# Kernel optimization log

Measured on AMD Instinct MI355X. Metric: run time of the kernel, lower is better.

## Reference

```python
import jax, jax.numpy as jnp
import numpy as np

RNN = 512        # rnn_units == embedding_units (required by LSTMCell input size)
ATT = 512        # attention_units
FEAT = 512       # feat_chans
VOCAB = 110
V1 = VOCAB + 1
MAX_LEN = 30
STEPS = MAX_LEN + 1
B, H, W = 32, 8, 32


def _lstm_cell(x, h, c, wih, whh, bih, bhh):
    # torch.nn.LSTMCell gate order: i, f, g, o
    gates = x @ wih.T + bih + h @ whh.T + bhh
    i, f, g, o = jnp.split(gates, 4, axis=-1)
    i, f, o = jax.nn.sigmoid(i), jax.nn.sigmoid(f), jax.nn.sigmoid(o)
    g = jnp.tanh(g)
    c_new = f * c + i * g
    h_new = o * jnp.tanh(c_new)
    return h_new, c_new


def setup_inputs() -> dict:
    key = jax.random.key(0)
    ks = jax.random.split(key, 16)
    s = 0.05

    def rn(k, shape):
        return jax.random.normal(k, shape, jnp.float32) * s

    return {
        "features": jax.random.normal(ks[0], (B, FEAT, H, W), jnp.float32),
        "holistic": jax.random.normal(ks[1], (B, RNN), jnp.float32),  # unused by forward (matches torch)
        "gt": jax.random.randint(ks[2], (B, STEPS), 0, V1),
        # AttentionModule params
        "W_feat": rn(ks[3], (ATT, FEAT, 3, 3)),
        "b_feat": jnp.zeros((ATT,), jnp.float32),
        "W_state": rn(ks[4], (ATT, RNN)),     # 1x1 conv, no bias
        "w_att": rn(ks[5], (ATT,)),           # 1x1 conv -> 1 channel, no bias
        # embedding (Linear, no bias): (embedding_units, vocab+1)
        "W_embed": rn(ks[6], (RNN, V1)),
        # LSTM cell 0
        "wih0": rn(ks[7], (4 * RNN, RNN)),
        "whh0": rn(ks[8], (4 * RNN, RNN)),
        "bih0": jnp.zeros((4 * RNN,), jnp.float32),
        "bhh0": jnp.zeros((4 * RNN,), jnp.float32),
        # LSTM cell 1
        "wih1": rn(ks[9], (4 * RNN, RNN)),
        "whh1": rn(ks[10], (4 * RNN, RNN)),
        "bih1": jnp.zeros((4 * RNN,), jnp.float32),
        "bhh1": jnp.zeros((4 * RNN,), jnp.float32),
        # output dense: (vocab+1, 2*rnn_units)
        "W_out": rn(ks[11], (V1, 2 * RNN)),
        "b_out": jnp.zeros((V1,), jnp.float32),
    }


def reference(features, holistic, gt, W_feat, b_feat, W_state, w_att, W_embed,
              wih0, whh0, bih0, bhh0, wih1, whh1, bih1, bhh1, W_out, b_out):
    Bsz, C, Hh, Ww = features.shape
    dt = features.dtype

    # feat_conv(features) is invariant across decode steps -> compute once
    feat_proj = jax.lax.conv_general_dilated(
        features, W_feat, window_strides=(1, 1), padding="SAME",
        dimension_numbers=("NCHW", "OIHW", "NCHW"),
    ) + b_feat[None, :, None, None]  # (B, ATT, H, W)

    # teacher-forced symbols: step 0 uses zeros, step t uses one_hot(gt[:, t-1])
    syms = jnp.concatenate(
        [jnp.zeros((Bsz, 1, V1), dt), jax.nn.one_hot(gt[:, :STEPS - 1], V1, dtype=dt)],
        axis=1,
    )
    syms = jnp.swapaxes(syms, 0, 1)  # (STEPS, B, V1)

    z = jnp.zeros((Bsz, RNN), dt)
    init = (z, z, z, z)  # h0, c0, h1, c1 (torch LSTMCell defaults to zero state)

    def step(carry, sym):
        h0, c0, h1, c1 = carry
        x = sym @ W_embed.T                                  # (B, RNN)
        h0, c0 = _lstm_cell(x, h0, c0, wih0, whh0, bih0, bhh0)
        h1, c1 = _lstm_cell(h0, h1, c1, wih1, whh1, bih1, bhh1)
        # attention glimpse: state is h1 broadcast as a 1x1 feature map
        sp = h1 @ W_state.T                                  # (B, ATT)
        proj = jnp.tanh(feat_proj + sp[:, :, None, None])    # (B, ATT, H, W)
        att = jnp.einsum("bahw,a->bhw", proj, w_att).reshape(Bsz, -1)
        att = jax.nn.softmax(att, axis=1).reshape(Bsz, Hh, Ww)
        glimpse = jnp.einsum("bchw,bhw->bc", features, att)  # (B, FEAT)
        logits = jnp.concatenate([h1, glimpse], axis=1) @ W_out.T + b_out
        return (h0, c0, h1, c1), logits

    _, logits = jax.lax.scan(step, init, syms)               # (STEPS, B, V1)
    return jnp.swapaxes(logits, 0, 1)                        # (B, STEPS, V1)
```

## Files before the change

kernel.cpp:

```cpp
#include <hip/hip_runtime.h>
#include <hip/hip_bf16.h>


#define RNN   512
#define V1    111
#define STEPS 31
#define HWP   256
#define NWG   128

typedef unsigned short ushortT;
typedef unsigned int   uintT;
typedef __attribute__((ext_vector_type(8))) short bf16x8;
typedef __attribute__((ext_vector_type(4))) float f32x4;

__device__ __forceinline__ float blo(uintT u){ union { uintT i; float f; } v; v.i = u << 16; return v.f; }
__device__ __forceinline__ float bhi(uintT u){ union { uintT i; float f; } v; v.i = u & 0xffff0000u; return v.f; }
__device__ __forceinline__ ushortT f2b(float f){
  __hip_bfloat16 h = __float2bfloat16(f);
  union { __hip_bfloat16 b; ushortT s; } v; v.b = h; return v.s;
}
__device__ __forceinline__ uintT packbf(float lo, float hi){
  return (uintT)f2b(lo) | ((uintT)f2b(hi) << 16);
}
__device__ __forceinline__ bf16x8 u4_to_b8(uint4 u){
  union { uint4 a; bf16x8 b; } v; v.a = u; return v.b;
}
__device__ __forceinline__ float sigf(float x){ return 1.f/(1.f + __expf(-x)); }
__device__ __forceinline__ float tanh_f(float x){ float e = __expf(2.f*x); return 1.f - 2.f/(e+1.f); }

__device__ __forceinline__ uintT sload_u(const uintT* p){
  return __hip_atomic_load((uintT*)p, __ATOMIC_RELAXED, __HIP_MEMORY_SCOPE_SYSTEM);
}
__device__ __forceinline__ void sstore_u(uintT* p, uintT v){
  __hip_atomic_store(p, v, __ATOMIC_RELAXED, __HIP_MEMORY_SCOPE_SYSTEM);
}
__device__ __forceinline__ void wait_ge(uintT* p, uintT tgt){
  for (;;){
    if (__hip_atomic_load(p, __ATOMIC_RELAXED, __HIP_MEMORY_SCOPE_SYSTEM) >= tgt) break;
    __builtin_amdgcn_s_sleep(2);
  }
}

__global__ __launch_bounds__(256) void k_pre(const float* __restrict__ feat,
                                             const float* __restrict__ Wf,
                                             uintT* __restrict__ fT,
                                             uintT* __restrict__ wb){
  const int bid = blockIdx.x, tid = threadIdx.x;
  if (bid < 10880){
    int idx = bid*256 + tid;
    int cp = idx & 255;
    int r  = idx >> 8;
    int xi = r % 34;
    int q  = r / 34;
    int yy = q % 10;
    int b  = q / 10;
    float v0 = 0.f, v1 = 0.f;
    if (yy >= 1 && yy <= 8 && xi >= 1 && xi <= 32){
      size_t base = (((size_t)b*512 + 2*cp)*8 + (yy-1))*32 + (xi-1);
      v0 = feat[base];
      v1 = feat[base + 256];
    }
    fT[idx] = packbf(v0, v1);
  } else {
    int idx = (bid - 10880)*256 + tid;
    int cp = idx & 255;
    int r  = idx >> 8;
    int a  = r & 511;
    int t  = r >> 9;
    float v0 = Wf[((size_t)a*512 + 2*cp)*9 + t];
    float v1 = Wf[((size_t)a*512 + 2*cp + 1)*9 + t];
    wb[idx] = packbf(v0, v1);
  }
}

__global__ __launch_bounds__(256) void k_post(
    const float* __restrict__ w0, const float* __restrict__ w1,
    const float* __restrict__ w2, uintT* __restrict__ wgb,
    const float* __restrict__ Wst, uintT* __restrict__ WstTb,
    const float* __restrict__ Wout, uintT* __restrict__ Woutb,
    const float* __restrict__ wih0, const float* __restrict__ Wemb,
    const float* __restrict__ bih0, const float* __restrict__ bhh0,
    float* __restrict__ M0,
    float* __restrict__ st, uintT* __restrict__ h1hist,
    uintT* __restrict__ h0hist, uintT* __restrict__ bar)
{
  const int bid = blockIdx.x, tid = threadIdx.x;
  if (bid < 6144){
    int idx = bid*256 + tid;
    int m = idx >> 19, r = idx & 524287;
    const float* s = (m==0)? w0 : (m==1)? w1 : w2;
    float2 v = *(const float2*)(s + 2*(size_t)r);
    wgb[idx] = packbf(v.x, v.y);
  } else if (bid < 6656){
    int idx = (bid-6144)*256 + tid;
    int u = idx >> 8, ap = idx & 255;
    WstTb[idx] = packbf(Wst[(size_t)(2*ap)*512 + u], Wst[(size_t)(2*ap+1)*512 + u]);
  } else if (bid < 6878){
    int idx = (bid-6656)*256 + tid;
    float2 v = *(const float2*)(Wout + 2*(size_t)idx);
    Woutb[idx] = packbf(v.x, v.y);
  } else if (bid < 7902){
    int j = (bid-6878)*2 + (tid >> 7);
    int g = tid & 127;
    float bs = bih0[j] + bhh0[j];
    if (g < V1){
      float a0=0.f, a1=0.f, a2=0.f, a3=0.f;
      const float* wr = wih0 + (size_t)j*512;
      for (int k=0;k<512;k+=4){
        a0 += wr[k]   * Wemb[(size_t)k*V1 + g];
        a1 += wr[k+1] * Wemb[(size_t)(k+1)*V1 + g];
        a2 += wr[k+2] * Wemb[(size_t)(k+2)*V1 + g];
        a3 += wr[k+3] * Wemb[(size_t)(k+3)*V1 + g];
      }
      M0[(size_t)j*112 + g] = ((a0+a1)+(a2+a3)) + bs;
    } else if (g == V1){
      M0[(size_t)j*112 + V1] = bs;
    }
  } else {
    int b2 = bid - 7902;
    if (b2 < 128)      st[b2*256 + tid] = 0.f;
    else if (b2 < 160) h1hist[(b2-128)*256 + tid] = 0u;
    else if (b2 < 192) h0hist[(b2-160)*256 + tid] = 0u;
    else               bar[(b2-192)*256 + tid] = 0u;
  }
}

__global__ __launch_bounds__(256) void k_convm(const ushortT* __restrict__ fT,
                                               const ushortT* __restrict__ wb,
                                               const float* __restrict__ bfv,
                                               ushortT* __restrict__ fpj)
{
  __shared__ __align__(16) ushortT a_lds[136*72];
  __shared__ __align__(16) ushortT b_lds[256*72];
  const int tid = threadIdx.x;
  const int w   = tid >> 6;
  const int l   = tid & 63;
  const int kg  = l >> 4;
  const int ln  = l & 15;
  const int bid = blockIdx.x;
  const int nh  = bid & 1;
  const int mt  = bid >> 1;
  const int b   = mt >> 2;
  const int y0  = (mt & 3) * 2;
  const int a0  = nh * 256;

  f32x4 acc[4][4];
  #pragma unroll
  for (int nb=0; nb<4; nb++){
    float bv = bfv[a0 + w*64 + nb*16 + ln];
    #pragma unroll
    for (int mb=0; mb<4; mb++){
      acc[mb][nb][0]=bv; acc[mb][nb][1]=bv; acc[mb][nb][2]=bv; acc[mb][nb][3]=bv;
    }
  }

  const char* aSrc = (const char*)(fT + (((size_t)b*10 + y0)*34)*512);
  const char* wSrc = (const char*)wb;

  for (int c0 = 0; c0 < 512; c0 += 64){
    {
      const char* s = aSrc + (size_t)c0*2;
      #pragma unroll
      for (int i=0;i<4;i++){
        int idx = tid + i*256;
        int pos = idx >> 3, q = idx & 7;
        uint4 v = *(const uint4*)(s + (size_t)pos*1024 + q*16);
        *(uint4*)((char*)a_lds + pos*144 + q*16) = v;
      }
      if (tid < 64){
        int idx = 1024 + tid;
        int pos = idx >> 3, q = idx & 7;
        uint4 v = *(const uint4*)(s + (size_t)pos*1024 + q*16);
        *(uint4*)((char*)a_lds + pos*144 + q*16) = v;
      }
    }
    #pragma unroll
    for (int t=0; t<9; t++){
      const int ky = t/3, kx = t - (t/3)*3;
      {
        const char* s = wSrc + (((size_t)t*512 + a0)*512 + c0)*2;
        #pragma unroll
        for (int i=0;i<8;i++){
          int idx = tid + i*256;
          int ai = idx >> 3, q = idx & 7;
          uint4 v = *(const uint4*)(s + (size_t)ai*1024 + q*16);
          *(uint4*)((char*)b_lds + ai*144 + q*16) = v;
        }
      }
      __syncthreads();
      #pragma unroll
      for (int ks=0; ks<2; ks++){
        bf16x8 afr[4], bfr[4];
        #pragma unroll
        for (int mb=0; mb<4; mb++){
          int row = ((mb>>1) + ky)*34 + (mb&1)*16 + ln + kx;
          afr[mb] = *(const bf16x8*)((const char*)a_lds + row*144 + kg*16 + ks*64);
        }
        #pragma unroll
        for (int nb=0; nb<4; nb++){
          int ai = w*64 + nb*16 + ln;
          bfr[nb] = *(const bf16x8*)((const char*)b_lds + ai*144 + kg*16 + ks*64);
        }
        #pragma unroll
        for (int mb=0; mb<4; mb++)
          #pragma unroll
          for (int nb=0; nb<4; nb++)
            acc[mb][nb] = __builtin_amdgcn_mfma_f32_16x16x32_bf16(afr[mb], bfr[nb], acc[mb][nb], 0, 0, 0);
      }
      __syncthreads();
    }
  }

  #pragma unroll
  for (int mb=0; mb<4; mb++){
    #pragma unroll
    for (int nb=0; nb<4; nb++){
      int a = a0 + w*64 + nb*16 + ln;
      #pragma unroll
      for (int r4=0; r4<4; r4++){
        int pos = mb*16 + kg*4 + r4;
        fpj[((size_t)b*HWP + (y0*32 + pos))*512 + a] = f2b(acc[mb][nb][r4]);
      }
    }
  }
}

__device__ __forceinline__ void stage_state_s(uintT* __restrict__ hs,
                                              const uintT* __restrict__ src, int tid){
  #pragma unroll
  for (int i=0;i<16;i++){
    int g = tid + i*512;
    hs[(g >> 8)*268 + (g & 255)] = sload_u(&src[g]);
  }
}

__global__ __launch_bounds__(512) void k_rec(
    const int* __restrict__ gt, const float* __restrict__ M0,
    const uintT* __restrict__ wgb,
    const float* __restrict__ bih1, const float* __restrict__ bhh1,
    float* __restrict__ st, uintT* __restrict__ h1hist,
    uintT* __restrict__ h0hist, uintT* __restrict__ bar)
{
  __shared__ __align__(16) float pool[19584];
  const int tid = threadIdx.x, bid = blockIdx.x;
  float* c0T = st;
  float* c1T = st + 16384;
  uintT* arrA = bar;
  uintT* arrB = bar + 1024;

  const bool isA = bid < 64;
  const int w   = tid >> 6;
  const int l   = tid & 63;
  const int kg  = l >> 4;
  const int ln  = l & 15;
  const int ks2 = w >> 2;
  const int rt  = (w >> 1) & 1;
  const int nh  = w & 1;
  const int u0  = (isA ? bid : bid - 64) * 8;
  const int jrow = (ln >> 2)*512 + u0 + rt*4 + (ln & 3);

  uintT* hs0 = (uintT*)pool;
  uintT* hs1 = (uintT*)pool + 8576;
  float* gs  = pool + 17152;
  float* hv  = pool + 19264;
  const ushortT* hb0 = (const ushortT*)hs0 + (nh*16 + ln)*536 + kg*8;
  const ushortT* hb1 = (const ushortT*)hs1 + (nh*16 + ln)*536 + kg*8;

  uint4 wA[8], wB[16];
  if (isA){
    const uintT* wp = wgb + (size_t)jrow*256 + kg*4;
    #pragma unroll
    for (int s8=0; s8<8; s8++) wA[s8] = *(const uint4*)(wp + (ks2*8 + s8)*16);
  } else {
    const uintT* wp = wgb + (ks2 ? 1048576 : 524288) + (size_t)jrow*256 + kg*4;
    #pragma unroll
    for (int s=0; s<16; s++) wB[s] = *(const uint4*)(wp + s*16);
  }

  for (int t = 0; t <= STEPS-1; t++){
    if (isA){
      if (t > 0){
        if (tid == 0) wait_ge(arrA + (t-1)*32, 64u);
        __syncthreads();
      }
      stage_state_s(hs0, h0hist + (size_t)t*8192, tid);
      __syncthreads();
      f32x4 acc = {0.f, 0.f, 0.f, 0.f};
      #pragma unroll
      for (int s8=0; s8<8; s8++){
        int s = ks2*8 + s8;
        bf16x8 bfr = *(const bf16x8*)(hb0 + s*32);
        acc = __builtin_amdgcn_mfma_f32_16x16x32_bf16(u4_to_b8(wA[s8]), bfr, acc, 0, 0, 0);
      }
      #pragma unroll
      for (int r=0;r<4;r++)
        gs[(ks2*32 + kg*8 + rt*4 + r)*33 + nh*16 + ln] = acc[r];
      __syncthreads();
      if (tid < 256){
        const int ul = tid >> 5, b = tid & 31, u = u0 + ul;
        float g4[4];
        #pragma unroll
        for (int g=0; g<4; g++){
          float sacc = gs[(g*8+ul)*33 + b] + gs[(32 + g*8+ul)*33 + b];
          int j = g*512 + u;
          int sym = (t > 0) ? gt[b*STEPS + t - 1] : V1;
          g4[g] = sacc + M0[(size_t)j*112 + sym];
        }
        int idx = u*32 + b;
        float cn = sigf(g4[1])*c0T[idx] + sigf(g4[0])*tanh_f(g4[2]);
        c0T[idx] = cn;
        hv[ul*33 + b] = sigf(g4[3])*tanh_f(cn);
      }
      __syncthreads();
      if (tid < 128){
        const int up = tid >> 5, b = tid & 31;
        sstore_u(&h0hist[(size_t)(t+1)*8192 + b*256 + (u0>>1) + up],
                 packbf(hv[(up*2)*33 + b], hv[(up*2+1)*33 + b]));
      }
      __syncthreads();
      if (tid == 0)
        __hip_atomic_fetch_add(arrA + t*32, 1u, __ATOMIC_RELAXED, __HIP_MEMORY_SCOPE_SYSTEM);
    } else {
      if (tid == 0){
        wait_ge(arrA + t*32, 64u);
        if (t > 0) wait_ge(arrB + (t-1)*32, 64u);
      }
      __syncthreads();
      stage_state_s(hs0, h0hist + (size_t)(t+1)*8192, tid);
      stage_state_s(hs1, h1hist + (size_t)t*8192, tid);
      __syncthreads();
      f32x4 acc = {0.f, 0.f, 0.f, 0.f};
      const ushortT* hbm = ks2 ? hb1 : hb0;
      #pragma unroll
      for (int s=0; s<16; s++){
        bf16x8 bfr = *(const bf16x8*)(hbm + s*32);
        acc = __builtin_amdgcn_mfma_f32_16x16x32_bf16(u4_to_b8(wB[s]), bfr, acc, 0, 0, 0);
      }
      #pragma unroll
      for (int r=0;r<4;r++)
        gs[(ks2*32 + kg*8 + rt*4 + r)*33 + nh*16 + ln] = acc[r];
      __syncthreads();
      if (tid < 256){
        const int ul = tid >> 5, b = tid & 31, u = u0 + ul;
        float g4[4];
        #pragma unroll
        for (int g=0; g<4; g++){
          float sacc = gs[(g*8+ul)*33 + b] + gs[(32 + g*8+ul)*33 + b];
          int j = g*512 + u;
          g4[g] = sacc + bih1[j] + bhh1[j];
        }
        int idx = u*32 + b;
        float cn = sigf(g4[1])*c1T[idx] + sigf(g4[0])*tanh_f(g4[2]);
        c1T[idx] = cn;
        hv[ul*33 + b] = sigf(g4[3])*tanh_f(cn);
      }
      __syncthreads();
      if (tid < 128){
        const int up = tid >> 5, b = tid & 31;
        sstore_u(&h1hist[(size_t)(t+1)*8192 + b*256 + (u0>>1) + up],
                 packbf(hv[(up*2)*33 + b], hv[(up*2+1)*33 + b]));
      }
      __syncthreads();
      if (tid == 0)
        __hip_atomic_fetch_add(arrB + t*32, 1u, __ATOMIC_RELAXED, __HIP_MEMORY_SCOPE_SYSTEM);
    }
  }
}

__global__ __launch_bounds__(512) void k_att(
    const float* __restrict__ features, const uintT* __restrict__ h1hist,
    const ushortT* __restrict__ fpj, const uintT* __restrict__ WstTb,
    const float* __restrict__ watt, const uintT* __restrict__ Woutb,
    const float* __restrict__ bout, float* __restrict__ out)
{
  __shared__ __align__(16) float pool[7488];
  const int tid = threadIdx.x;
  const int b = blockIdx.x / STEPS, r = blockIdx.x % STEPS;
  float* h1s   = pool;
  float* spsl  = pool + 512;
  float* watts = pool + 1024;
  float* pals  = pool + 1536;
  float* attw  = pool + 2048;
  float* glim  = pool + 2304;
  float* red   = pool + 2816;
  float* opart = pool + 2880;
  float* sppt  = pool + 3392;

  if (tid < 256){
    uintT hvw = h1hist[(size_t)(r+1)*8192 + b*256 + tid];
    h1s[2*tid]   = blo(hvw);
    h1s[2*tid+1] = bhi(hvw);
  }
  watts[tid] = watt[tid];
  __syncthreads();

  {
    int ap4 = tid & 63, uq = tid >> 6;
    float a8[8] = {0.f,0.f,0.f,0.f,0.f,0.f,0.f,0.f};
    const uint4* wp = (const uint4*)(WstTb + (size_t)(uq*64)*256) + ap4;
    const float* hq = h1s + uq*64;
    #pragma unroll 8
    for (int u=0; u<64; u++){
      uint4 q = wp[(size_t)u*64];
      float h = hq[u];
      a8[0] += blo(q.x)*h; a8[1] += bhi(q.x)*h;
      a8[2] += blo(q.y)*h; a8[3] += bhi(q.y)*h;
      a8[4] += blo(q.z)*h; a8[5] += bhi(q.z)*h;
      a8[6] += blo(q.w)*h; a8[7] += bhi(q.w)*h;
    }
    #pragma unroll
    for (int j=0;j<8;j++) sppt[uq*512 + ap4*8 + j] = a8[j];
  }
  __syncthreads();
  {
    float s = 0.f;
    #pragma unroll
    for (int uq=0;uq<8;uq++) s += sppt[uq*512 + tid];
    spsl[tid] = s;
  }
  __syncthreads();

  {
    int p = tid & 255, ac = tid >> 8;
    const uint4* fr = (const uint4*)(fpj + ((size_t)b*HWP + p)*512 + ac*256);
    float al2 = 0.f;
    #pragma unroll 8
    for (int kb=0;kb<32;kb++){
      uint4 q = fr[kb];
      float v[8] = {blo(q.x),bhi(q.x),blo(q.y),bhi(q.y),blo(q.z),bhi(q.z),blo(q.w),bhi(q.w)};
      int a0 = ac*256 + kb*8;
      #pragma unroll
      for (int i=0;i<8;i++)
        al2 += watts[a0+i] * tanh_f(v[i] + spsl[a0+i]);
    }
    pals[tid] = al2;
  }
  __syncthreads();
  {
    float al2 = (tid < 256) ? (pals[tid] + pals[256+tid]) : -1e30f;
    float m = al2;
    #pragma unroll
    for (int off=32; off>0; off>>=1) m = fmaxf(m, __shfl_xor(m, off));
    if (tid < 256 && (tid & 63)==0) red[tid>>6] = m;
    __syncthreads();
    m = fmaxf(fmaxf(red[0],red[1]), fmaxf(red[2],red[3]));
    float e = (tid < 256) ? __expf(al2 - m) : 0.f;
    float s = e;
    #pragma unroll
    for (int off=32; off>0; off>>=1) s += __shfl_xor(s, off);
    __syncthreads();
    if (tid < 256 && (tid & 63)==0) red[tid>>6] = s;
    __syncthreads();
    if (tid < 256){
      float sa = red[0]+red[1]+red[2]+red[3];
      attw[tid] = e / sa;
    }
  }
  __syncthreads();
  {
    const float4* fr = (const float4*)(features + ((size_t)b*512 + tid)*256);
    float acc = 0.f;
    #pragma unroll 8
    for (int kb=0;kb<64;kb++){
      float4 v = fr[kb];
      const float* aw = attw + kb*4;
      acc += v.x*aw[0] + v.y*aw[1] + v.z*aw[2] + v.w*aw[3];
    }
    glim[tid] = acc;
  }
  __syncthreads();
  {
    int q = tid >> 7, o = tid & 127;
    float acc = 0.f;
    if (o < V1){
      const uint4* wr4 = (const uint4*)(Woutb + (size_t)o*512 + q*128);
      const float* src = (q < 2) ? (h1s + q*256) : (glim + (q-2)*256);
      #pragma unroll 8
      for (int kb=0;kb<32;kb++){
        uint4 w4 = wr4[kb];
        const float* sx = src + kb*8;
        acc += blo(w4.x)*sx[0] + bhi(w4.x)*sx[1] + blo(w4.y)*sx[2] + bhi(w4.y)*sx[3]
             + blo(w4.z)*sx[4] + bhi(w4.z)*sx[5] + blo(w4.w)*sx[6] + bhi(w4.w)*sx[7];
      }
    }
    opart[tid] = acc;
  }
  __syncthreads();
  if (tid < V1){
    float acc = bout[tid] + opart[tid] + opart[128+tid] + opart[256+tid] + opart[384+tid];
    out[(size_t)b*STEPS*V1 + (size_t)r*V1 + tid] = acc;
  }
}

extern "C" void kernel_launch(void* const* d_in, const int* in_sizes, int n_in,
                              void* d_out, int out_size, void* d_ws, size_t ws_size,
                              hipStream_t stream)
{
  const float* features = (const float*)d_in[0];
  const int*   gt       = (const int*)d_in[2];
  const float* Wf    = (const float*)d_in[3];
  const float* bfv   = (const float*)d_in[4];
  const float* Wst   = (const float*)d_in[5];
  const float* watt  = (const float*)d_in[6];
  const float* Wemb  = (const float*)d_in[7];
  const float* wih0  = (const float*)d_in[8];
  const float* whh0  = (const float*)d_in[9];
  const float* bih0  = (const float*)d_in[10];
  const float* bhh0  = (const float*)d_in[11];
  const float* wih1  = (const float*)d_in[12];
  const float* whh1  = (const float*)d_in[13];
  const float* bih1  = (const float*)d_in[14];
  const float* bhh1  = (const float*)d_in[15];
  const float* Wout  = (const float*)d_in[16];
  const float* bout  = (const float*)d_in[17];
  float* out = (float*)d_out;

  char* wsb = (char*)d_ws;
  ushortT* fpj    = (ushortT*)(wsb + 0);
  uintT*   h1hist = (uintT*)  (wsb + 8388608);
  uintT*   h0hist = (uintT*)  (wsb + 9437184);
  float*   M0     = (float*)  (wsb + 16777216);
  uintT*   wgb    = (uintT*)  (wsb + 17694720);
  uintT*   Woutb  = (uintT*)  (wsb + 23986176);
  uintT*   WstTb  = (uintT*)  (wsb + 24215552);
  float*   st     = (float*)  (wsb + 24739840);
  uintT*   bar    = (uintT*)  (wsb + 24936448);
  uintT*   fTt    = (uintT*)  (wsb + 8388608);
  ushortT* wbt    = (ushortT*)(wsb + 19529728);

  k_pre  <<<15488, 256, 0, stream>>>(features, Wf, fTt, (uintT*)wbt);
  k_convm<<<256,   256, 0, stream>>>((const ushortT*)fTt, wbt, bfv, fpj);
  k_post <<<8102,  256, 0, stream>>>(whh0, wih1, whh1, wgb,
                                     Wst, WstTb, Wout, Woutb,
                                     wih0, Wemb, bih0, bhh0, M0,
                                     st, h1hist, h0hist, bar);
  k_rec  <<<NWG,   512, 0, stream>>>(gt, M0, wgb, bih1, bhh1, st,
                                     h1hist, h0hist, bar);
  k_att  <<<32*STEPS, 512, 0, stream>>>(features, h1hist, fpj, WstTb, watt,
                                        Woutb, bout, out);
  (void)in_sizes; (void)n_in; (void)out_size; (void)ws_size;
}
```

Measured before the change: 673.7 us.

## Fold weight-prep kernel into recurrent kernel with grid gate; keep cell state in registers

Removes the separate k_post launch and does its weight conversion, M0 precompute and history zeroing at the start of the persistent k_rec kernel. A grid-wide atomic gate then makes all workgroups wait until that prep is done. The LSTM cell state now lives in a register per thread instead of being read and written in global memory each step. Barrier arrivals switch to release ordering. This saves one launch and the per-step global c traffic, but the prep work now runs on only 128 workgroups instead of thousands of blocks.

Measured after the change: 756.8 us. +12.3%, slower.

```diff
diff --git a/kernel.cpp b/kernel.cpp
--- a/kernel.cpp
+++ b/kernel.cpp
@@ -34,17 +34,25 @@
 __device__ __forceinline__ void sstore_u(uintT* p, uintT v){
   __hip_atomic_store(p, v, __ATOMIC_RELAXED, __HIP_MEMORY_SCOPE_SYSTEM);
 }
+__device__ __forceinline__ void sstore_f(float* p, float v){
+  __hip_atomic_store(p, v, __ATOMIC_RELAXED, __HIP_MEMORY_SCOPE_SYSTEM);
+}
 __device__ __forceinline__ void wait_ge(uintT* p, uintT tgt){
   for (;;){
     if (__hip_atomic_load(p, __ATOMIC_RELAXED, __HIP_MEMORY_SCOPE_SYSTEM) >= tgt) break;
     __builtin_amdgcn_s_sleep(2);
   }
 }
+__device__ __forceinline__ void arrive_rel(uintT* p){
+  __hip_atomic_fetch_add(p, 1u, __ATOMIC_RELEASE, __HIP_MEMORY_SCOPE_SYSTEM);
+}
 
 __global__ __launch_bounds__(256) void k_pre(const float* __restrict__ feat,
                                              const float* __restrict__ Wf,
                                              uintT* __restrict__ fT,
-                                             uintT* __restrict__ wb){
+                                             uintT* __restrict__ wb,
+                                             uintT* __restrict__ bar,
+                                             uintT* __restrict__ gate){
   const int bid = blockIdx.x, tid = threadIdx.x;
   if (bid < 10880){
     int idx = bid*256 + tid;
@@ -61,7 +69,7 @@
       v1 = feat[base + 256];
     }
     fT[idx] = packbf(v0, v1);
-  } else {
+  } else if (bid < 15488){
     int idx = (bid - 10880)*256 + tid;
     int cp = idx & 255;
     int r  = idx >> 8;
@@ -70,58 +78,10 @@
     float v0 = Wf[((size_t)a*512 + 2*cp)*9 + t];
     float v1 = Wf[((size_t)a*512 + 2*cp + 1)*9 + t];
     wb[idx] = packbf(v0, v1);
-  }
-}
-
-__global__ __launch_bounds__(256) void k_post(
-    const float* __restrict__ w0, const float* __restrict__ w1,
-    const float* __restrict__ w2, uintT* __restrict__ wgb,
-    const float* __restrict__ Wst, uintT* __restrict__ WstTb,
-    const float* __restrict__ Wout, uintT* __restrict__ Woutb,
-    const float* __restrict__ wih0, const float* __restrict__ Wemb,
-    const float* __restrict__ bih0, const float* __restrict__ bhh0,
-    float* __restrict__ M0,
-    float* __restrict__ st, uintT* __restrict__ h1hist,
-    uintT* __restrict__ h0hist, uintT* __restrict__ bar)
-{
-  const int bid = blockIdx.x, tid = threadIdx.x;
-  if (bid < 6144){
-    int idx = bid*256 + tid;
-    int m = idx >> 19, r = idx & 524287;
-    const float* s = (m==0)? w0 : (m==1)? w1 : w2;
-    float2 v = *(const float2*)(s + 2*(size_t)r);
-    wgb[idx] = packbf(v.x, v.y);
-  } else if (bid < 6656){
-    int idx = (bid-6144)*256 + tid;
-    int u = idx >> 8, ap = idx & 255;
-    WstTb[idx] = packbf(Wst[(size_t)(2*ap)*512 + u], Wst[(size_t)(2*ap+1)*512 + u]);
-  } else if (bid < 6878){
-    int idx = (bid-6656)*256 + tid;
-    float2 v = *(const float2*)(Wout + 2*(size_t)idx);
-    Woutb[idx] = packbf(v.x, v.y);
-  } else if (bid < 7902){
-    int j = (bid-6878)*2 + (tid >> 7);
-    int g = tid & 127;
-    float bs = bih0[j] + bhh0[j];
-    if (g < V1){
-      float a0=0.f, a1=0.f, a2=0.f, a3=0.f;
-      const float* wr = wih0 + (size_t)j*512;
-      for (int k=0;k<512;k+=4){
-        a0 += wr[k]   * Wemb[(size_t)k*V1 + g];
-        a1 += wr[k+1] * Wemb[(size_t)(k+1)*V1 + g];
-        a2 += wr[k+2] * Wemb[(size_t)(k+2)*V1 + g];
-        a3 += wr[k+3] * Wemb[(size_t)(k+3)*V1 + g];
-      }
-      M0[(size_t)j*112 + g] = ((a0+a1)+(a2+a3)) + bs;
-    } else if (g == V1){
-      M0[(size_t)j*112 + V1] = bs;
-    }
   } else {
-    int b2 = bid - 7902;
-    if (b2 < 128)      st[b2*256 + tid] = 0.f;
-    else if (b2 < 160) h1hist[(b2-128)*256 + tid] = 0u;
-    else if (b2 < 192) h0hist[(b2-160)*256 + tid] = 0u;
-    else               bar[(b2-192)*256 + tid] = 0u;
+    #pragma unroll
+    for (int i=0;i<8;i++) sstore_u(&bar[tid + i*256], 0u);
+    if (tid == 0) sstore_u(gate, 0u);
   }
 }
 
@@ -235,18 +195,67 @@
 }
 
 __global__ __launch_bounds__(512) void k_rec(
-    const int* __restrict__ gt, const float* __restrict__ M0,
-    const uintT* __restrict__ wgb,
+    const int* __restrict__ gt,
+    const float* __restrict__ whh0, const float* __restrict__ wih1,
+    const float* __restrict__ whh1, uintT* __restrict__ wgb,
+    const float* __restrict__ Wst, uintT* __restrict__ WstTb,
+    const float* __restrict__ Wout, uintT* __restrict__ Woutb,
+    const float* __restrict__ wih0, const float* __restrict__ Wemb,
+    const float* __restrict__ bih0, const float* __restrict__ bhh0,
+    float* __restrict__ M0,
     const float* __restrict__ bih1, const float* __restrict__ bhh1,
-    float* __restrict__ st, uintT* __restrict__ h1hist,
-    uintT* __restrict__ h0hist, uintT* __restrict__ bar)
+    uintT* __restrict__ h1hist, uintT* __restrict__ h0hist,
+    uintT* __restrict__ bar, uintT* __restrict__ gate)
 {
   __shared__ __align__(16) float pool[19584];
   const int tid = threadIdx.x, bid = blockIdx.x;
-  float* c0T = st;
-  float* c1T = st + 16384;
   uintT* arrA = bar;
   uintT* arrB = bar + 1024;
+
+  {
+    const int gid = bid*512 + tid;
+    for (int i = gid; i < 1572864; i += 65536){
+      int m = i >> 19, r = i & 524287;
+      const float* s = (m==0)? whh0 : (m==1)? wih1 : whh1;
+      float2 v = *(const float2*)(s + 2*(size_t)r);
+      sstore_u(&wgb[i], packbf(v.x, v.y));
+    }
+    for (int i = gid; i < 131072; i += 65536){
+      int u = i >> 8, ap = i & 255;
+      sstore_u(&WstTb[i], packbf(Wst[(size_t)(2*ap)*512 + u], Wst[(size_t)(2*ap+1)*512 + u]));
+    }
+    if (gid < 56832){
+      float2 v = *(const float2*)(Wout + 2*(size_t)gid);
+      sstore_u(&Woutb[gid], packbf(v.x, v.y));
+    }
+    for (int i = gid; i < 262144; i += 65536){
+      int j = i >> 7, g = i & 127;
+      float bs = bih0[j] + bhh0[j];
+      if (g < V1){
+        float a0=0.f, a1=0.f, a2=0.f, a3=0.f;
+        const float* wr = wih0 + (size_t)j*512;
+        for (int k=0;k<512;k+=4){
+          a0 += wr[k]   * Wemb[(size_t)k*V1 + g];
+          a1 += wr[k+1] * Wemb[(size_t)(k+1)*V1 + g];
+          a2 += wr[k+2] * Wemb[(size_t)(k+2)*V1 + g];
+          a3 += wr[k+3] * Wemb[(size_t)(k+3)*V1 + g];
+        }
+        sstore_f(&M0[(size_t)j*112 + g], ((a0+a1)+(a2+a3)) + bs);
+      } else if (g == V1){
+        sstore_f(&M0[(size_t)j*112 + V1], bs);
+      }
+    }
+    if (gid < 8192){
+      sstore_u(&h0hist[gid], 0u);
+      sstore_u(&h1hist[gid], 0u);
+    }
+    __syncthreads();
+    if (tid == 0){
+      arrive_rel(gate);
+      wait_ge(gate, (uintT)NWG);
+    }
+    __syncthreads();
+  }
 
   const bool isA = bid < 64;
   const int w   = tid >> 6;
@@ -277,6 +286,8 @@
     for (int s=0; s<16; s++) wB[s] = *(const uint4*)(wp + s*16);
   }
 
+  float creg = 0.f;
+
   for (int t = 0; t <= STEPS-1; t++){
     if (isA){
       if (t > 0){
@@ -306,9 +317,8 @@
           int sym = (t > 0) ? gt[b*STEPS + t - 1] : V1;
           g4[g] = sacc + M0[(size_t)j*112 + sym];
         }
-        int idx = u*32 + b;
-        float cn = sigf(g4[1])*c0T[idx] + sigf(g4[0])*tanh_f(g4[2]);
-        c0T[idx] = cn;
+        float cn = sigf(g4[1])*creg + sigf(g4[0])*tanh_f(g4[2]);
+        creg = cn;
         hv[ul*33 + b] = sigf(g4[3])*tanh_f(cn);
       }
       __syncthreads();
@@ -318,8 +328,7 @@
                  packbf(hv[(up*2)*33 + b], hv[(up*2+1)*33 + b]));
       }
       __syncthreads();
-      if (tid == 0)
-        __hip_atomic_fetch_add(arrA + t*32, 1u, __ATOMIC_RELAXED, __HIP_MEMORY_SCOPE_SYSTEM);
+      if (tid == 0) arrive_rel(arrA + t*32);
     } else {
       if (tid == 0){
         wait_ge(arrA + t*32, 64u);
@@ -349,9 +358,8 @@
           int j = g*512 + u;
           g4[g] = sacc + bih1[j] + bhh1[j];
         }
-        int idx = u*32 + b;
-        float cn = sigf(g4[1])*c1T[idx] + sigf(g4[0])*tanh_f(g4[2]);
-        c1T[idx] = cn;
+        float cn = sigf(g4[1])*creg + sigf(g4[0])*tanh_f(g4[2]);
+        creg = cn;
         hv[ul*33 + b] = sigf(g4[3])*tanh_f(cn);
       }
       __syncthreads();
@@ -361,8 +369,7 @@
                  packbf(hv[(up*2)*33 + b], hv[(up*2+1)*33 + b]));
       }
       __syncthreads();
-      if (tid == 0)
-        __hip_atomic_fetch_add(arrB + t*32, 1u, __ATOMIC_RELAXED, __HIP_MEMORY_SCOPE_SYSTEM);
+      if (tid == 0) arrive_rel(arrB + t*32);
     }
   }
 }
@@ -523,19 +530,17 @@
   uintT*   wgb    = (uintT*)  (wsb + 17694720);
   uintT*   Woutb  = (uintT*)  (wsb + 23986176);
   uintT*   WstTb  = (uintT*)  (wsb + 24215552);
-  float*   st     = (float*)  (wsb + 24739840);
+  uintT*   gate   = (uintT*)  (wsb + 24739840);
   uintT*   bar    = (uintT*)  (wsb + 24936448);
   uintT*   fTt    = (uintT*)  (wsb + 8388608);
   ushortT* wbt    = (ushortT*)(wsb + 19529728);
 
-  k_pre  <<<15488, 256, 0, stream>>>(features, Wf, fTt, (uintT*)wbt);
+  k_pre  <<<15489, 256, 0, stream>>>(features, Wf, fTt, (uintT*)wbt, bar, gate);
   k_convm<<<256,   256, 0, stream>>>((const ushortT*)fTt, wbt, bfv, fpj);
-  k_post <<<8102,  256, 0, stream>>>(whh0, wih1, whh1, wgb,
+  k_rec  <<<NWG,   512, 0, stream>>>(gt, whh0, wih1, whh1, wgb,
                                      Wst, WstTb, Wout, Woutb,
                                      wih0, Wemb, bih0, bhh0, M0,
-                                     st, h1hist, h0hist, bar);
-  k_rec  <<<NWG,   512, 0, stream>>>(gt, M0, wgb, bih1, bhh1, st,
-                                     h1hist, h0hist, bar);
+                                     bih1, bhh1, h1hist, h0hist, bar, gate);
   k_att  <<<32*STEPS, 512, 0, stream>>>(features, h1hist, fpj, WstTb, watt,
                                         Woutb, bout, out);
   (void)in_sizes; (void)n_in; (void)out_size; (void)ws_size;
```
